# Optimization experiments

Measured on AMD Instinct MI355X. Metric: run time of the kernel, lower is better.

Reference implementation:

```python
import jax, jax.numpy as jnp
import numpy as np

B, L, C = 2, 4096, 1024
H, WIN = 16, 128            # num_heads, window_size (each side)
D = C // H                  # head_dim = 64


def setup_inputs() -> dict:
    key = jax.random.key(0)
    ks = jax.random.split(key, 9)
    s = 0.02
    return {
        "x": jax.random.normal(ks[0], (B, L, C), jnp.float32),
        # Linear weights stored as [in, out] (y = x @ W + b), same math as torch Linear.
        "wq": jax.random.normal(ks[1], (C, C), jnp.float32) * s,
        "bq": jnp.zeros((C,), jnp.float32),
        "wk": jax.random.normal(ks[2], (C, C), jnp.float32) * s,
        "bk": jnp.zeros((C,), jnp.float32),
        "wv": jax.random.normal(ks[3], (C, C), jnp.float32) * s,
        "bv": jnp.zeros((C,), jnp.float32),
        "wo": jax.random.normal(ks[4], (C, C), jnp.float32) * s,
        "bo": jnp.zeros((C,), jnp.float32),
    }


def reference(x, wq, bq, wk, bk, wv, bv, wo, bo):
    b, l, c = x.shape
    nb = l // WIN

    def heads(t):  # (B,L,C) -> (B,H,L,D)
        return t.reshape(b, l, H, D).transpose(0, 2, 1, 3)

    q = heads(x @ wq + bq)
    k = heads(x @ wk + bk)
    v = heads(x @ wv + bv)

    # and ARE included in the softmax, exactly as the original module does).
    kp = jnp.pad(k, ((0, 0), (0, 0), (WIN, WIN), (0, 0)))
    vp = jnp.pad(v, ((0, 0), (0, 0), (WIN, WIN), (0, 0)))

    idx = np.arange(nb)[:, None] * WIN + np.arange(3 * WIN)[None, :]  # [nb, 3W]
    kb = kp[:, :, idx]  # [B,H,nb,3W,D]
    vb = vp[:, :, idx]  # [B,H,nb,3W,D]
    qb = q.reshape(b, H, nb, WIN, D)

    scores = jnp.einsum('bhnqd,bhnkd->bhnqk', qb, kb) / float(np.sqrt(D))
    r = np.arange(WIN)[:, None]
    col = np.arange(3 * WIN)[None, :]
    band = jnp.asarray(np.abs(col - r - WIN) <= WIN)
    scores = jnp.where(band, scores, -jnp.inf)
    probs = jax.nn.softmax(scores, axis=-1)

    out = jnp.einsum('bhnqk,bhnkd->bhnqd', probs, vb)
    out = out.reshape(b, H, l, D).transpose(0, 2, 1, 3).reshape(b, l, c)
    return out @ wo + bo
```

## Files before the change

### kernel.cpp

```cpp
#include <hip/hip_runtime.h>

using short8  = __attribute__((ext_vector_type(8))) short;
using short4v = __attribute__((ext_vector_type(4))) short;
using floatx4 = __attribute__((ext_vector_type(4))) float;

#define MFMA_B16(a, b, c) __builtin_amdgcn_mfma_f32_16x16x32_bf16(a, b, c, 0, 0, 0)

__device__ __forceinline__ short f2bf(float f) {
  union { float f; unsigned u; } v; v.f = f;
  unsigned r = v.u + 0x7fffu + ((v.u >> 16) & 1u);
  return (short)(r >> 16);
}
__device__ __forceinline__ short f2bf_rtz(float f) {
  union { float f; unsigned u; } v; v.f = f;
  return (short)(v.u >> 16);
}

__device__ __forceinline__ void gload_lds16(const short* g, short* l) {
  __builtin_amdgcn_global_load_lds(
      (const __attribute__((address_space(1))) unsigned int*)g,
      (__attribute__((address_space(3))) unsigned int*)l, 16, 0, 0);
}

__global__ __launch_bounds__(256) void prep(
    const float4* __restrict__ x, short4v* __restrict__ xb,
    const float* __restrict__ w0, const float* __restrict__ w1,
    const float* __restrict__ w2, const float* __restrict__ w3,
    short* __restrict__ wT) {
  __shared__ float tile[32][33];
  int blk = blockIdx.x;
  if (blk < 8192) {
    int i = blk * 256 + threadIdx.x;
    float4 v = x[i];
    short4v o = { f2bf(v.x), f2bf(v.y), f2bf(v.z), f2bf(v.w) };
    xb[i] = o;
  } else {
    int r = blk - 8192;
    int z = r >> 10; r &= 1023;
    const float* w = z == 0 ? w0 : (z == 1 ? w1 : (z == 2 ? w2 : w3));
    short* out = wT + (size_t)z * 1024 * 1024;
    int n0 = (r & 31) * 32, k0 = (r >> 5) * 32;
    int tx = threadIdx.x & 31, ty = threadIdx.x >> 5;
#pragma unroll
    for (int i = 0; i < 4; ++i)
      tile[ty + i * 8][tx] = w[(size_t)(k0 + ty + i * 8) * 1024 + n0 + tx];
    __syncthreads();
#pragma unroll
    for (int i = 0; i < 4; ++i)
      out[(size_t)(n0 + ty + i * 8) * 1024 + k0 + tx] = f2bf(tile[tx][ty + i * 8]);
  }
}

__device__ __forceinline__ void gemm_core_256x128(
    const short* __restrict__ Ag0, const short* __restrict__ Bg0,
    short* As , short* Bs ,
    floatx4 (&acc)[8][2]) {
  const int tid = threadIdx.x;
  const int w = tid >> 6, lane = tid & 63, quad = lane >> 4, l16 = lane & 15;
  const int wm = w >> 2, wn = w & 3;
  const int srow = tid >> 3;
  const int scol = ((tid & 7) ^ (srow & 7)) * 8;

  floatx4 zf = {0.f, 0.f, 0.f, 0.f};
#pragma unroll
  for (int i = 0; i < 8; ++i) { acc[i][0] = zf; acc[i][1] = zf; }

  const short* gA = Ag0 + (size_t)srow * 1024 + scol;
  const short* gB = Bg0 + (size_t)srow * 1024 + scol;

  auto stA = [&](int buf, int q, int kt) {
    gload_lds16(gA + (size_t)q * 64 * 1024 + kt * 64,
                As + buf * 16384 + q * 4096 + w * 512);
  };
  auto stB = [&](int buf, int q, int kt) {
    gload_lds16(gB + (size_t)q * 64 * 1024 + kt * 64,
                Bs + buf * 8192 + q * 4096 + w * 512);
  };

  short8 aF[8], bF[4];
  auto ldA = [&](int buf, int mh) {
    const char* base = (const char*)(As + buf * 16384);
#pragma unroll
    for (int m = 0; m < 4; ++m)
#pragma unroll
      for (int kk = 0; kk < 2; ++kk) {
        int row = wm * 128 + mh * 64 + m * 16 + l16;
        int off = row * 128 + kk * 64 + quad * 16;
        off ^= (row & 7) << 4;
        aF[m * 2 + kk] = *(const short8*)(base + off);
      }
  };
  auto ldB = [&](int buf) {
    const char* base = (const char*)(Bs + buf * 8192);
#pragma unroll
    for (int nf = 0; nf < 2; ++nf)
#pragma unroll
      for (int kk = 0; kk < 2; ++kk) {
        int row = wn * 32 + nf * 16 + l16;
        int off = row * 128 + kk * 64 + quad * 16;
        off ^= (row & 7) << 4;
        bF[nf * 2 + kk] = *(const short8*)(base + off);
      }
  };
  auto mm = [&](int mh) {
#pragma unroll
    for (int m = 0; m < 4; ++m)
#pragma unroll
      for (int nf = 0; nf < 2; ++nf)
#pragma unroll
        for (int kk = 0; kk < 2; ++kk)
          acc[mh * 4 + m][nf] =
              MFMA_B16(aF[m * 2 + kk], bF[nf * 2 + kk], acc[mh * 4 + m][nf]);
  };

  stA(0, 0, 0); stA(0, 1, 0); stA(0, 2, 0); stA(0, 3, 0);
  stB(0, 0, 0); stB(0, 1, 0);
  stA(1, 0, 1); stA(1, 2, 1); stB(1, 0, 1);
  asm volatile("s_waitcnt vmcnt(3)" ::: "memory");
  __builtin_amdgcn_s_barrier();

#pragma unroll 2
  for (int t = 0; t < 16; ++t) {
    const int cb = t & 1, nb = cb ^ 1;
    ldA(cb, 0);
    ldB(cb);
    if (t + 1 < 16) { stA(nb, 1, t + 1); stA(nb, 3, t + 1); stB(nb, 1, t + 1); }
    __builtin_amdgcn_sched_barrier(0);
    __builtin_amdgcn_s_barrier();
    asm volatile("s_waitcnt lgkmcnt(0)" ::: "memory");
    __builtin_amdgcn_sched_barrier(0);
    __builtin_amdgcn_s_setprio(1);
    mm(0);
    __builtin_amdgcn_s_setprio(0);
    __builtin_amdgcn_sched_barrier(0);
    __builtin_amdgcn_s_barrier();
    ldA(cb, 1);
    if (t + 2 < 16) {
      stA(cb, 0, t + 2); stA(cb, 2, t + 2); stB(cb, 0, t + 2);
      asm volatile("s_waitcnt vmcnt(3)" ::: "memory");
    } else {
      asm volatile("s_waitcnt vmcnt(0)" ::: "memory");
    }
    __builtin_amdgcn_sched_barrier(0);
    __builtin_amdgcn_s_barrier();
    asm volatile("s_waitcnt lgkmcnt(0)" ::: "memory");
    __builtin_amdgcn_sched_barrier(0);
    __builtin_amdgcn_s_setprio(1);
    mm(1);
    __builtin_amdgcn_s_setprio(0);
    __builtin_amdgcn_sched_barrier(0);
    __builtin_amdgcn_s_barrier();
  }
}

__global__ __launch_bounds__(512, 2) void gemm_qkv(
    const short* __restrict__ xb, const short* __restrict__ wT,
    const float* __restrict__ bq, const float* __restrict__ bk,
    const float* __restrict__ bv, short* __restrict__ qkv) {
  __shared__ __align__(16) short As[2 * 16384];
  __shared__ __align__(16) short Bs[2 * 8192];
  int z = blockIdx.z;
  const short* wt = wT + (size_t)z * 1024 * 1024;
  const float* bias = z == 0 ? bq : (z == 1 ? bk : bv);
  short* out = qkv + (size_t)z * 8192 * 1024;
  int m0 = blockIdx.x * 256, n0 = blockIdx.y * 128;

  floatx4 acc[8][2];
  gemm_core_256x128(xb + (size_t)m0 * 1024, wt + (size_t)n0 * 1024, As, Bs, acc);

  int tid = threadIdx.x, w = tid >> 6, lane = tid & 63, quad = lane >> 4, l16 = lane & 15;
  int wm = w >> 2, wn = w & 3;
  float qs = (z == 0) ? 0.125f * 1.44269504f : 1.0f;
#pragma unroll
  for (int mf = 0; mf < 8; ++mf)
#pragma unroll
    for (int nf = 0; nf < 2; ++nf)
#pragma unroll
      for (int rg = 0; rg < 4; ++rg) {
        int m = m0 + wm * 128 + mf * 16 + quad * 4 + rg;
        int cc = n0 + wn * 32 + nf * 16 + l16;
        float v = (acc[mf][nf][rg] + bias[cc]) * qs;
        int b = m >> 12, l = m & 4095;
        int hh = cc >> 6, d = cc & 63;
        out[((size_t)(b * 16 + hh) * 4096 + l) * 64 + d] = f2bf(v);
      }
}

__global__ __launch_bounds__(256) void attn_kern(const short* __restrict__ qkv,
                                                 short* __restrict__ attnb) {
  const int L = 4096, H = 16;
  int n = blockIdx.x, h = blockIdx.y, b = blockIdx.z;
  const size_t hs = (size_t)L * 64;
  const short* Qp = qkv + (size_t)(b * H + h) * hs;
  const short* Kp = qkv + (size_t)8192 * 1024 + (size_t)(b * H + h) * hs;
  const short* Vp = qkv + (size_t)2 * 8192 * 1024 + (size_t)(b * H + h) * hs;

  __shared__ __align__(16) short kt[128][72];
  __shared__ __align__(16) short vt[64][136];
  __shared__ __align__(16) short pl[4][32][136];

  int tid = threadIdx.x, w = tid >> 6, lane = tid & 63, quad = lane >> 4, l16 = lane & 15;

  short8 onesf;
  {
    short ov = (l16 == 0) ? (short)0x3F80 : (short)0;
#pragma unroll
    for (int j = 0; j < 8; ++j) onesf[j] = ov;
  }

  short8 qf[2][2];
#pragma unroll
  for (int rt = 0; rt < 2; ++rt)
#pragma unroll
    for (int ks = 0; ks < 2; ++ks)
      qf[rt][ks] = *(const short8*)(Qp + (size_t)(n * 128 + w * 32 + rt * 16 + l16) * 64 + ks * 32 + quad * 8);

  floatx4 zf = {0.f, 0.f, 0.f, 0.f};
  floatx4 o[2][4];
  floatx4 osum[2];
#pragma unroll
  for (int i = 0; i < 2; ++i) {
    osum[i] = zf;
#pragma unroll
    for (int j = 0; j < 4; ++j) o[i][j] = zf;
  }

#pragma unroll
  for (int c = 0; c < 3; ++c) {
    int bk = n - 1 + c;
    bool inr = (c == 1) || (c == 0 ? (n > 0) : (n < 31));
    __syncthreads();
    if (inr) {
      const short* kc_ = Kp + (size_t)bk * 128 * 64;
      int kr = tid >> 2, ksg = (tid & 3) * 16;
#pragma unroll
      for (int p = 0; p < 2; ++p) {
        int r2 = p * 64 + kr;
        *(short8*)(&kt[r2][ksg])     = *(const short8*)(kc_ + r2 * 64 + ksg);
        *(short8*)(&kt[r2][ksg + 8]) = *(const short8*)(kc_ + r2 * 64 + ksg + 8);
      }
      const short* vc_ = Vp + (size_t)bk * 128 * 64;
      int vkey = tid & 31, vsg = (tid >> 5) * 8;
#pragma unroll
      for (int p = 0; p < 4; ++p) {
        int r2 = p * 32 + vkey;
        short8 vv = *(const short8*)(vc_ + r2 * 64 + vsg);
#pragma unroll
        for (int j = 0; j < 8; ++j) vt[vsg + j][r2] = vv[j];
      }
    } else {
      short8 z8 = {0, 0, 0, 0, 0, 0, 0, 0};
      int kr = tid >> 2, ksg = (tid & 3) * 16;
#pragma unroll
      for (int p = 0; p < 2; ++p) {
        int r2 = p * 64 + kr;
        *(short8*)(&kt[r2][ksg])     = z8;
        *(short8*)(&kt[r2][ksg + 8]) = z8;
      }
      int vr = tid >> 2, vsg2 = (tid & 3) * 32;
#pragma unroll
      for (int q2 = 0; q2 < 4; ++q2) *(short8*)(&vt[vr][vsg2 + q2 * 8]) = z8;
    }
    __syncthreads();

    floatx4 s[2][8];
#pragma unroll
    for (int rt = 0; rt < 2; ++rt)
#pragma unroll
      for (int ct = 0; ct < 8; ++ct) s[rt][ct] = zf;
#pragma unroll
    for (int ct = 0; ct < 8; ++ct) {
      bool any = (c == 0) ? (ct >= w * 2) : (c == 2) ? (ct <= w * 2 + 1) : true;
      if (any) {
        short8 kf0 = *(const short8*)(&kt[ct * 16 + l16][quad * 8]);
        short8 kf1 = *(const short8*)(&kt[ct * 16 + l16][32 + quad * 8]);
#pragma unroll
        for (int rt = 0; rt < 2; ++rt) {
          bool valid = (c == 0) ? (ct >= w * 2 + rt) : (c == 2) ? (ct <= w * 2 + rt) : true;
          if (valid) {
            s[rt][ct] = MFMA_B16(qf[rt][0], kf0, s[rt][ct]);
            s[rt][ct] = MFMA_B16(qf[rt][1], kf1, s[rt][ct]);
          }
        }
      }
    }

#pragma unroll
    for (int rt = 0; rt < 2; ++rt) {
      int wrt = w * 2 + rt;
#pragma unroll
      for (int ct = 0; ct < 8; ++ct) {
        bool tileMasked = (c == 0) ? (ct < wrt) : (c == 2) ? (ct > wrt) : false;
        bool ksDead = (c == 0) ? (2 * (ct >> 1) + 1 < wrt)
                    : (c == 2) ? (2 * (ct >> 1) > wrt) : false;
        bool diag = (c != 1) && (ct == wrt);
        if (ksDead) continue;
        if (tileMasked) {
#pragma unroll
          for (int rg = 0; rg < 4; ++rg)
            pl[w][rt * 16 + quad * 4 + rg][ct * 16 + l16] = 0;
        } else if (diag) {
#pragma unroll
          for (int rg = 0; rg < 4; ++rg) {
            int r16 = quad * 4 + rg;
            float p = exp2f(s[rt][ct][rg]);
            if (c == 0) p = (l16 < r16) ? 0.f : p;
            else        p = (l16 > r16) ? 0.f : p;
            pl[w][rt * 16 + r16][ct * 16 + l16] = f2bf_rtz(p);
          }
        } else {
#pragma unroll
          for (int rg = 0; rg < 4; ++rg)
            pl[w][rt * 16 + quad * 4 + rg][ct * 16 + l16] = f2bf_rtz(exp2f(s[rt][ct][rg]));
        }
      }
    }

    __syncthreads();

#pragma unroll
    for (int ks = 0; ks < 4; ++ks) {
      bool anyrt = (c == 0) ? (2 * ks + 1 >= w * 2) : (c == 2) ? (2 * ks <= w * 2 + 1) : true;
      if (!anyrt) continue;
      short8 vf[4];
#pragma unroll
      for (int ct = 0; ct < 4; ++ct)
        vf[ct] = *(const short8*)(&vt[ct * 16 + l16][ks * 32 + quad * 8]);
#pragma unroll
      for (int rt = 0; rt < 2; ++rt) {
        int wrt = w * 2 + rt;
        bool ksDead = (c == 0) ? (2 * ks + 1 < wrt) : (c == 2) ? (2 * ks > wrt) : false;
        if (ksDead) continue;
        short8 pf = *(const short8*)(&pl[w][rt * 16 + l16][ks * 32 + quad * 8]);
#pragma unroll
        for (int ct = 0; ct < 4; ++ct) o[rt][ct] = MFMA_B16(pf, vf[ct], o[rt][ct]);
        osum[rt] = MFMA_B16(pf, onesf, osum[rt]);
      }
    }
  }

#pragma unroll
  for (int rt = 0; rt < 2; ++rt) {
#pragma unroll
    for (int rg = 0; rg < 4; ++rg) {
      float ssum = __shfl(osum[rt][rg], lane & 48);
      float inv = 1.f / ssum;
      int r = n * 128 + w * 32 + rt * 16 + quad * 4 + rg;
#pragma unroll
      for (int ct = 0; ct < 4; ++ct)
        attnb[(size_t)(b * L + r) * 1024 + h * 64 + ct * 16 + l16] =
            f2bf(o[rt][ct][rg] * inv);
    }
  }
}

__global__ __launch_bounds__(512, 2) void gemm_out(
    const short* __restrict__ attnb, const short* __restrict__ wTo,
    const float* __restrict__ bo, float* __restrict__ outp) {
  __shared__ __align__(16) short As[2 * 16384];
  __shared__ __align__(16) short Bs[2 * 8192];
  int m0 = blockIdx.x * 256, n0 = blockIdx.y * 128;

  floatx4 acc[8][2];
  gemm_core_256x128(attnb + (size_t)m0 * 1024, wTo + (size_t)n0 * 1024, As, Bs, acc);

  int tid = threadIdx.x, w = tid >> 6, lane = tid & 63, quad = lane >> 4, l16 = lane & 15;
  int wm = w >> 2, wn = w & 3;
#pragma unroll
  for (int mf = 0; mf < 8; ++mf)
#pragma unroll
    for (int nf = 0; nf < 2; ++nf)
#pragma unroll
      for (int rg = 0; rg < 4; ++rg) {
        int m = m0 + wm * 128 + mf * 16 + quad * 4 + rg;
        int cc = n0 + wn * 32 + nf * 16 + l16;
        outp[(size_t)m * 1024 + cc] = acc[mf][nf][rg] + bo[cc];
      }
}

extern "C" void kernel_launch(void* const* d_in, const int* in_sizes, int n_in,
                              void* d_out, int out_size, void* d_ws, size_t ws_size,
                              hipStream_t stream) {
  const float* x  = (const float*)d_in[0];
  const float* wq = (const float*)d_in[1];
  const float* bq = (const float*)d_in[2];
  const float* wk = (const float*)d_in[3];
  const float* bk = (const float*)d_in[4];
  const float* wv = (const float*)d_in[5];
  const float* bv = (const float*)d_in[6];
  const float* wo = (const float*)d_in[7];
  const float* bo = (const float*)d_in[8];

  char* ws = (char*)d_ws;
  short* xb    = (short*)ws;
  short* wT    = (short*)(ws + (16u << 20));
  short* qkv   = (short*)(ws + (24u << 20));
  short* attnb = (short*)(ws + (72u << 20));

  prep<<<12288, 256, 0, stream>>>((const float4*)x, (short4v*)xb, wq, wk, wv, wo, wT);
  gemm_qkv<<<dim3(32, 8, 3), 512, 0, stream>>>(xb, wT, bq, bk, bv, qkv);
  attn_kern<<<dim3(32, 16, 2), 256, 0, stream>>>(qkv, attnb);
  gemm_out<<<dim3(32, 8), 512, 0, stream>>>(attnb, wT + 3u * 1024 * 1024, bo, (float*)d_out);
}
```

Before: 226.8 us.

## Enlarge projection GEMM tiles to 256x256 with four-phase pipelined K loop

Both projection GEMMs now compute 256x256 output tiles instead of 256x128. Each wave holds a 128x64 accumulator, and the K loop is split into four MFMA phases that interleave LDS fragment loads with staggered global-to-LDS prefetches. This raises arithmetic intensity and cuts redundant A-tile loads from global memory. The cost is a doubled B buffer in LDS (128KB total per block) and more accumulator registers. Grid sizes are halved to 384 and 128 blocks, which lowers occupancy and may underfill 256 CUs, especially in gemm_out.

```diff
diff --git a/kernel.cpp b/kernel.cpp
--- a/kernel.cpp
+++ b/kernel.cpp
@@ -51,10 +51,10 @@
   }
 }
 
-__device__ __forceinline__ void gemm_core_256x128(
+__device__ __forceinline__ void gemm_core_256x256(
     const short* __restrict__ Ag0, const short* __restrict__ Bg0,
     short* As , short* Bs ,
-    floatx4 (&acc)[8][2]) {
+    floatx4 (&acc)[8][4]) {
   const int tid = threadIdx.x;
   const int w = tid >> 6, lane = tid & 63, quad = lane >> 4, l16 = lane & 15;
   const int wm = w >> 2, wn = w & 3;
@@ -63,7 +63,9 @@
 
   floatx4 zf = {0.f, 0.f, 0.f, 0.f};
 #pragma unroll
-  for (int i = 0; i < 8; ++i) { acc[i][0] = zf; acc[i][1] = zf; }
+  for (int i = 0; i < 8; ++i)
+#pragma unroll
+    for (int j = 0; j < 4; ++j) acc[i][j] = zf;
 
   const short* gA = Ag0 + (size_t)srow * 1024 + scol;
   const short* gB = Bg0 + (size_t)srow * 1024 + scol;
@@ -74,10 +76,10 @@
   };
   auto stB = [&](int buf, int q, int kt) {
     gload_lds16(gB + (size_t)q * 64 * 1024 + kt * 64,
-                Bs + buf * 8192 + q * 4096 + w * 512);
+                Bs + buf * 16384 + q * 4096 + w * 512);
   };
 
-  short8 aF[8], bF[4];
+  short8 aF[8], bF[8];
   auto ldA = [&](int buf, int mh) {
     const char* base = (const char*)(As + buf * 16384);
 #pragma unroll
@@ -90,63 +92,83 @@
         aF[m * 2 + kk] = *(const short8*)(base + off);
       }
   };
-  auto ldB = [&](int buf) {
-    const char* base = (const char*)(Bs + buf * 8192);
-#pragma unroll
-    for (int nf = 0; nf < 2; ++nf)
+  auto ldB = [&](int buf, int nh) {
+    const char* base = (const char*)(Bs + buf * 16384);
+#pragma unroll
+    for (int n = 0; n < 2; ++n)
 #pragma unroll
       for (int kk = 0; kk < 2; ++kk) {
-        int row = wn * 32 + nf * 16 + l16;
+        int row = wn * 64 + nh * 32 + n * 16 + l16;
         int off = row * 128 + kk * 64 + quad * 16;
         off ^= (row & 7) << 4;
-        bF[nf * 2 + kk] = *(const short8*)(base + off);
+        bF[(nh * 2 + n) * 2 + kk] = *(const short8*)(base + off);
       }
   };
-  auto mm = [&](int mh) {
+  auto mm = [&](int mh, int nh) {
 #pragma unroll
     for (int m = 0; m < 4; ++m)
 #pragma unroll
-      for (int nf = 0; nf < 2; ++nf)
+      for (int n = 0; n < 2; ++n)
 #pragma unroll
         for (int kk = 0; kk < 2; ++kk)
-          acc[mh * 4 + m][nf] =
-              MFMA_B16(aF[m * 2 + kk], bF[nf * 2 + kk], acc[mh * 4 + m][nf]);
+          acc[mh * 4 + m][nh * 2 + n] =
+              MFMA_B16(aF[m * 2 + kk], bF[(nh * 2 + n) * 2 + kk],
+                       acc[mh * 4 + m][nh * 2 + n]);
   };
 
   stA(0, 0, 0); stA(0, 1, 0); stA(0, 2, 0); stA(0, 3, 0);
-  stB(0, 0, 0); stB(0, 1, 0);
-  stA(1, 0, 1); stA(1, 2, 1); stB(1, 0, 1);
-  asm volatile("s_waitcnt vmcnt(3)" ::: "memory");
+  stB(0, 0, 0); stB(0, 1, 0); stB(0, 2, 0); stB(0, 3, 0);
+  stA(1, 0, 1); stA(1, 2, 1);
+  stB(1, 0, 1); stB(1, 1, 1); stB(1, 2, 1); stB(1, 3, 1);
+  asm volatile("s_waitcnt vmcnt(6)" ::: "memory");
   __builtin_amdgcn_s_barrier();
 
 #pragma unroll 2
   for (int t = 0; t < 16; ++t) {
     const int cb = t & 1, nb = cb ^ 1;
     ldA(cb, 0);
-    ldB(cb);
-    if (t + 1 < 16) { stA(nb, 1, t + 1); stA(nb, 3, t + 1); stB(nb, 1, t + 1); }
+    ldB(cb, 0);
+    if (t + 1 < 16) { stA(nb, 1, t + 1); stA(nb, 3, t + 1); }
     __builtin_amdgcn_sched_barrier(0);
     __builtin_amdgcn_s_barrier();
     asm volatile("s_waitcnt lgkmcnt(0)" ::: "memory");
     __builtin_amdgcn_sched_barrier(0);
     __builtin_amdgcn_s_setprio(1);
-    mm(0);
+    mm(0, 0);
     __builtin_amdgcn_s_setprio(0);
     __builtin_amdgcn_sched_barrier(0);
     __builtin_amdgcn_s_barrier();
+    ldB(cb, 1);
+    if (t + 2 < 16) { stA(cb, 0, t + 2); stA(cb, 2, t + 2); }
+    __builtin_amdgcn_sched_barrier(0);
+    __builtin_amdgcn_s_barrier();
+    asm volatile("s_waitcnt lgkmcnt(0)" ::: "memory");
+    __builtin_amdgcn_sched_barrier(0);
+    __builtin_amdgcn_s_setprio(1);
+    mm(0, 1);
+    __builtin_amdgcn_s_setprio(0);
+    __builtin_amdgcn_sched_barrier(0);
+    __builtin_amdgcn_s_barrier();
     ldA(cb, 1);
+    if (t + 2 < 16) { stB(cb, 0, t + 2); stB(cb, 1, t + 2); }
+    __builtin_amdgcn_sched_barrier(0);
+    __builtin_amdgcn_s_barrier();
+    asm volatile("s_waitcnt lgkmcnt(0)" ::: "memory");
+    __builtin_amdgcn_sched_barrier(0);
+    __builtin_amdgcn_s_setprio(1);
+    mm(1, 0);
+    __builtin_amdgcn_s_setprio(0);
+    __builtin_amdgcn_sched_barrier(0);
+    __builtin_amdgcn_s_barrier();
     if (t + 2 < 16) {
-      stA(cb, 0, t + 2); stA(cb, 2, t + 2); stB(cb, 0, t + 2);
-      asm volatile("s_waitcnt vmcnt(3)" ::: "memory");
+      stB(cb, 2, t + 2); stB(cb, 3, t + 2);
+      asm volatile("s_waitcnt vmcnt(6)" ::: "memory");
     } else {
       asm volatile("s_waitcnt vmcnt(0)" ::: "memory");
     }
     __builtin_amdgcn_sched_barrier(0);
-    __builtin_amdgcn_s_barrier();
-    asm volatile("s_waitcnt lgkmcnt(0)" ::: "memory");
-    __builtin_amdgcn_sched_barrier(0);
     __builtin_amdgcn_s_setprio(1);
-    mm(1);
+    mm(1, 1);
     __builtin_amdgcn_s_setprio(0);
     __builtin_amdgcn_sched_barrier(0);
     __builtin_amdgcn_s_barrier();
@@ -158,15 +180,15 @@
     const float* __restrict__ bq, const float* __restrict__ bk,
     const float* __restrict__ bv, short* __restrict__ qkv) {
   __shared__ __align__(16) short As[2 * 16384];
-  __shared__ __align__(16) short Bs[2 * 8192];
+  __shared__ __align__(16) short Bs[2 * 16384];
   int z = blockIdx.z;
   const short* wt = wT + (size_t)z * 1024 * 1024;
   const float* bias = z == 0 ? bq : (z == 1 ? bk : bv);
   short* out = qkv + (size_t)z * 8192 * 1024;
-  int m0 = blockIdx.x * 256, n0 = blockIdx.y * 128;
-
-  floatx4 acc[8][2];
-  gemm_core_256x128(xb + (size_t)m0 * 1024, wt + (size_t)n0 * 1024, As, Bs, acc);
+  int m0 = blockIdx.x * 256, n0 = blockIdx.y * 256;
+
+  floatx4 acc[8][4];
+  gemm_core_256x256(xb + (size_t)m0 * 1024, wt + (size_t)n0 * 1024, As, Bs, acc);
 
   int tid = threadIdx.x, w = tid >> 6, lane = tid & 63, quad = lane >> 4, l16 = lane & 15;
   int wm = w >> 2, wn = w & 3;
@@ -174,11 +196,11 @@
 #pragma unroll
   for (int mf = 0; mf < 8; ++mf)
 #pragma unroll
-    for (int nf = 0; nf < 2; ++nf)
+    for (int nf = 0; nf < 4; ++nf)
 #pragma unroll
       for (int rg = 0; rg < 4; ++rg) {
         int m = m0 + wm * 128 + mf * 16 + quad * 4 + rg;
-        int cc = n0 + wn * 32 + nf * 16 + l16;
+        int cc = n0 + wn * 64 + nf * 16 + l16;
         float v = (acc[mf][nf][rg] + bias[cc]) * qs;
         int b = m >> 12, l = m & 4095;
         int hh = cc >> 6, d = cc & 63;
@@ -358,22 +380,22 @@
     const short* __restrict__ attnb, const short* __restrict__ wTo,
     const float* __restrict__ bo, float* __restrict__ outp) {
   __shared__ __align__(16) short As[2 * 16384];
-  __shared__ __align__(16) short Bs[2 * 8192];
-  int m0 = blockIdx.x * 256, n0 = blockIdx.y * 128;
-
-  floatx4 acc[8][2];
-  gemm_core_256x128(attnb + (size_t)m0 * 1024, wTo + (size_t)n0 * 1024, As, Bs, acc);
+  __shared__ __align__(16) short Bs[2 * 16384];
+  int m0 = blockIdx.x * 256, n0 = blockIdx.y * 256;
+
+  floatx4 acc[8][4];
+  gemm_core_256x256(attnb + (size_t)m0 * 1024, wTo + (size_t)n0 * 1024, As, Bs, acc);
 
   int tid = threadIdx.x, w = tid >> 6, lane = tid & 63, quad = lane >> 4, l16 = lane & 15;
   int wm = w >> 2, wn = w & 3;
 #pragma unroll
   for (int mf = 0; mf < 8; ++mf)
 #pragma unroll
-    for (int nf = 0; nf < 2; ++nf)
+    for (int nf = 0; nf < 4; ++nf)
 #pragma unroll
       for (int rg = 0; rg < 4; ++rg) {
         int m = m0 + wm * 128 + mf * 16 + quad * 4 + rg;
-        int cc = n0 + wn * 32 + nf * 16 + l16;
+        int cc = n0 + wn * 64 + nf * 16 + l16;
         outp[(size_t)m * 1024 + cc] = acc[mf][nf][rg] + bo[cc];
       }
 }
@@ -398,7 +420,7 @@
   short* attnb = (short*)(ws + (72u << 20));
 
   prep<<<12288, 256, 0, stream>>>((const float4*)x, (short4v*)xb, wq, wk, wv, wo, wT);
-  gemm_qkv<<<dim3(32, 8, 3), 512, 0, stream>>>(xb, wT, bq, bk, bv, qkv);
+  gemm_qkv<<<dim3(32, 4, 3), 512, 0, stream>>>(xb, wT, bq, bk, bv, qkv);
   attn_kern<<<dim3(32, 16, 2), 256, 0, stream>>>(qkv, attnb);
-  gemm_out<<<dim3(32, 8), 512, 0, stream>>>(attnb, wT + 3u * 1024 * 1024, bo, (float*)d_out);
-}
+  gemm_out<<<dim3(32, 4), 512, 0, stream>>>(attnb, wT + 3u * 1024 * 1024, bo, (float*)d_out);
+}
```

New measurement: 233.1 us. +2.8%, slower.
